# Performance work log

Measured on AMD Instinct MI355X. Metric: run time of the kernel, lower is better.

Reference implementation:

```python
import jax, jax.numpy as jnp
import numpy as np

N = 100000   # nodes
E = 1600000  # edges (avg degree 16)
D = 64       # input_dim
H = 64       # hidden_dim
C = 40       # num_classes
K = 2        # x_steps (KProp)


def setup_inputs() -> dict:
    key = jax.random.key(0)
    ks = jax.random.split(key, 8)
    x = jax.random.normal(ks[0], (N, D), dtype=jnp.float32)
    edge_src = jax.random.randint(ks[1], (E,), 0, N, dtype=jnp.int32)
    edge_dst = jax.random.randint(ks[2], (E,), 0, N, dtype=jnp.int32)
    def lin(k, fi, fo):
        b = 1.0 / np.sqrt(fi)
        return jax.random.uniform(k, (fi, fo), jnp.float32, -b, b)
    Wl1 = lin(ks[3], D, H)  # SAGEConv1 neighbor weight
    Wr1 = lin(ks[4], D, H)  # SAGEConv1 root weight
    b1 = jnp.zeros((H,), jnp.float32)
    Wl2 = lin(ks[5], H, C)
    Wr2 = lin(ks[6], H, C)
    b2 = jnp.zeros((C,), jnp.float32)
    return {"x": x, "Wl1": Wl1, "Wr1": Wr1, "b1": b1,
            "Wl2": Wl2, "Wr2": Wr2, "b2": b2,
            "edge_src": edge_src, "edge_dst": edge_dst}


def reference(x, Wl1, Wr1, b1, Wl2, Wr2, b2, edge_src, edge_dst):
    ones = jnp.ones((edge_src.shape[0],), x.dtype)
    deg = jax.ops.segment_sum(ones, edge_dst, num_segments=N)  # in-degree (adj_t row sums)
    # gcn_norm without self loops: w_e = deg[dst]^-1/2 * deg[src]^-1/2 (inf -> 0)
    dis = jnp.where(deg > 0, jax.lax.rsqrt(jnp.maximum(deg, 1.0)), 0.0)
    w = dis[edge_dst] * dis[edge_src]
    # KProp: K steps of normalized sparse matmul, 'add' aggregation
    h = x
    for _ in range(K):
        h = jax.ops.segment_sum(h[edge_src] * w[:, None], edge_dst, num_segments=N)
    cnt = jnp.maximum(deg, 1.0)[:, None]  # mean-aggr denominator (0-row safe)
    # SAGEConv1: lin_l(mean_neighbors) + lin_r(root), then selu (dropout p=0)
    agg1 = jax.ops.segment_sum(h[edge_src], edge_dst, num_segments=N) / cnt
    h1 = jax.nn.selu(agg1 @ Wl1 + h @ Wr1 + b1)
    # SAGEConv2
    agg2 = jax.ops.segment_sum(h1[edge_src], edge_dst, num_segments=N) / cnt
    out = agg2 @ Wl2 + h1 @ Wr2 + b2
    return jax.nn.softmax(out, axis=1)
```

## Files before the change

kernel.cpp:

```cpp
#include <hip/hip_runtime.h>
#include <hip/hip_bf16.h>
#include <math.h>


#define RFL(x) __builtin_amdgcn_readfirstlane(x)
#define BK_SHIFT 10
#define MAXBUCK 256

__device__ __forceinline__ float bf2f(unsigned short u) {
    return __uint_as_float((unsigned)u << 16);
}


__global__ void init_bcursor_kernel(int* __restrict__ bcursor, int nbuck, int cap) {
    int i = blockIdx.x * blockDim.x + threadIdx.x;
    if (i < nbuck) bcursor[i] = i * cap;
}

__global__ __launch_bounds__(256) void partition_kernel(const int* __restrict__ src,
                                                        const int* __restrict__ dst,
                                                        int* __restrict__ bcursor,
                                                        unsigned int* __restrict__ temp,
                                                        int e, int nbuck, int cap) {
    __shared__ int bc[MAXBUCK];
    int t = threadIdx.x;
    int chunk = (e + gridDim.x - 1) / gridDim.x;
    int base = blockIdx.x * chunk;
    int cnt = e - base;
    if (cnt > chunk) cnt = chunk;
    if (cnt < 0) cnt = 0;
    for (int j = t; j < nbuck; j += 256) bc[j] = 0;
    __syncthreads();
    for (int i = t; i < cnt; i += 256) {
        int d = dst[base + i];
        atomicAdd(&bc[d >> BK_SHIFT], 1);
    }
    __syncthreads();
    for (int j = t; j < nbuck; j += 256) {
        int c = bc[j];
        bc[j] = (c > 0) ? atomicAdd(&bcursor[j], c) : 0;
    }
    __syncthreads();
    for (int i = t; i < cnt; i += 256) {
        int s = src[base + i];
        int d = dst[base + i];
        int bk = d >> BK_SHIFT;
        int p = atomicAdd(&bc[bk], 1);
        if (p < (bk + 1) * cap) temp[p] = ((unsigned int)s << BK_SHIFT) | (unsigned int)(d & 1023);
    }
}

__global__ __launch_bounds__(256) void bucket_csr_kernel(const unsigned int* __restrict__ temp,
                                                         const int* __restrict__ bcursor,
                                                         int* __restrict__ row_ptr,
                                                         float* __restrict__ dis,
                                                         float* __restrict__ cnt_inv,
                                                         int* __restrict__ csr_src,
                                                         int n, int cap, int nbuck, int e) {
    __shared__ int cnt3[1024];
    __shared__ int part[256];
    int b = blockIdx.x;
    int t = threadIdx.x;
    int nbeg = b << BK_SHIFT;
    int cj = 0;
    if (t < nbuck) {
        cj = bcursor[t] - t * cap;
        if (cj > cap) cj = cap;
    }
    part[t] = cj;
    __syncthreads();
    for (int off = 1; off < 256; off <<= 1) {
        int u = (t >= off) ? part[t - off] : 0;
        __syncthreads();
        part[t] += u;
        __syncthreads();
    }
    int cntb = bcursor[b] - b * cap;
    if (cntb > cap) cntb = cap;
    int bbase = part[b] - cntb;
    __syncthreads();
    for (int i = t; i < 1024; i += 256) cnt3[i] = 0;
    __syncthreads();
    const unsigned int* tb = temp + (size_t)b * cap;
    for (int i = t; i < cntb; i += 256) {
        atomicAdd(&cnt3[tb[i] & 1023u], 1);
    }
    __syncthreads();
    int d0 = cnt3[t * 4 + 0], d1 = cnt3[t * 4 + 1], d2 = cnt3[t * 4 + 2], d3 = cnt3[t * 4 + 3];
    int run = d0 + d1 + d2 + d3;
    int dd[4] = {d0, d1, d2, d3};
#pragma unroll
    for (int k = 0; k < 4; ++k) {
        int node = nbeg + t * 4 + k;
        if (node < n) {
            float fd = (float)dd[k];
            dis[node] = (dd[k] > 0) ? rsqrtf(fd) : 0.0f;
            cnt_inv[node] = 1.0f / fmaxf(fd, 1.0f);
        }
    }
    __syncthreads();
    part[t] = run;
    __syncthreads();
    for (int off = 1; off < 256; off <<= 1) {
        int u = (t >= off) ? part[t - off] : 0;
        __syncthreads();
        part[t] += u;
        __syncthreads();
    }
    int ex = part[t] - run;
    int oo[4];
    oo[0] = ex; oo[1] = ex + d0; oo[2] = ex + d0 + d1; oo[3] = ex + d0 + d1 + d2;
#pragma unroll
    for (int k = 0; k < 4; ++k) {
        cnt3[t * 4 + k] = oo[k];
        int node = nbeg + t * 4 + k;
        if (node < n) row_ptr[node] = bbase + oo[k];
    }
    if (b == nbuck - 1 && t == 0) row_ptr[n] = e;
    __syncthreads();
    for (int i = t; i < cntb; i += 256) {
        unsigned int ed = tb[i];
        int pos = atomicAdd(&cnt3[ed & 1023u], 1);
        csr_src[bbase + pos] = (int)(ed >> BK_SHIFT);
    }
}

template <int TAG>
__global__ __launch_bounds__(256) void prop4_kernel(const float4* __restrict__ in4,
                                                    float4* __restrict__ out4,
                                                    const int* __restrict__ row_ptr,
                                                    const int* __restrict__ csr_src,
                                                    const float* __restrict__ dis,
                                                    int n) {
    int lane = threadIdx.x & 63;
    int g = lane >> 4;
    int l = lane & 15;
    int node = RFL(blockIdx.x * 4 + (threadIdx.x >> 6));
    if (node >= n) return;
    int beg = row_ptr[node];
    int end = row_ptr[node + 1];
    float4 acc = make_float4(0.f, 0.f, 0.f, 0.f);
    int j = beg;
    for (; j + 16 <= end; j += 16) {
        int s[4];
        float4 v[4];
        float w[4];
#pragma unroll
        for (int q = 0; q < 4; ++q) s[q] = csr_src[j + q * 4 + g];
#pragma unroll
        for (int q = 0; q < 4; ++q) v[q] = in4[(size_t)s[q] * 16 + l];
#pragma unroll
        for (int q = 0; q < 4; ++q) w[q] = dis[s[q]];
#pragma unroll
        for (int q = 0; q < 4; ++q) {
            acc.x += w[q] * v[q].x;
            acc.y += w[q] * v[q].y;
            acc.z += w[q] * v[q].z;
            acc.w += w[q] * v[q].w;
        }
    }
    for (; j + 8 <= end; j += 8) {
        int s[2];
        float4 v[2];
        float w[2];
#pragma unroll
        for (int q = 0; q < 2; ++q) s[q] = csr_src[j + q * 4 + g];
#pragma unroll
        for (int q = 0; q < 2; ++q) v[q] = in4[(size_t)s[q] * 16 + l];
#pragma unroll
        for (int q = 0; q < 2; ++q) w[q] = dis[s[q]];
#pragma unroll
        for (int q = 0; q < 2; ++q) {
            acc.x += w[q] * v[q].x;
            acc.y += w[q] * v[q].y;
            acc.z += w[q] * v[q].z;
            acc.w += w[q] * v[q].w;
        }
    }
    for (; j < end; j += 4) {
        int idx = j + g;
        bool valid = idx < end;
        int s = csr_src[valid ? idx : (end - 1)];
        float w = valid ? dis[s] : 0.0f;
        float4 v = in4[(size_t)s * 16 + l];
        acc.x += w * v.x;
        acc.y += w * v.y;
        acc.z += w * v.z;
        acc.w += w * v.w;
    }
    acc.x += __shfl_xor(acc.x, 16); acc.x += __shfl_xor(acc.x, 32);
    acc.y += __shfl_xor(acc.y, 16); acc.y += __shfl_xor(acc.y, 32);
    acc.z += __shfl_xor(acc.z, 16); acc.z += __shfl_xor(acc.z, 32);
    acc.w += __shfl_xor(acc.w, 16); acc.w += __shfl_xor(acc.w, 32);
    if (g == 0) {
        float sc = dis[node];
        out4[(size_t)node * 16 + l] = make_float4(acc.x * sc, acc.y * sc, acc.z * sc, acc.w * sc);
    }
}

__global__ __launch_bounds__(256) void prop_mean_bf_kernel(const ushort4* __restrict__ in4u,
                                                           float4* __restrict__ out4,
                                                           const int* __restrict__ row_ptr,
                                                           const int* __restrict__ csr_src,
                                                           const float* __restrict__ cnt_inv,
                                                           const float4* __restrict__ r4,
                                                           const float4* __restrict__ b4,
                                                           int n) {
    int lane = threadIdx.x & 63;
    int g = lane >> 4;
    int l = lane & 15;
    int node = RFL(blockIdx.x * 4 + (threadIdx.x >> 6));
    if (node >= n) return;
    int beg = row_ptr[node];
    int end = row_ptr[node + 1];
    float4 acc = make_float4(0.f, 0.f, 0.f, 0.f);
    int j = beg;
    for (; j + 16 <= end; j += 16) {
        int s[4];
        ushort4 u[4];
#pragma unroll
        for (int q = 0; q < 4; ++q) s[q] = csr_src[j + q * 4 + g];
#pragma unroll
        for (int q = 0; q < 4; ++q) u[q] = in4u[(size_t)s[q] * 16 + l];
#pragma unroll
        for (int q = 0; q < 4; ++q) {
            acc.x += bf2f(u[q].x);
            acc.y += bf2f(u[q].y);
            acc.z += bf2f(u[q].z);
            acc.w += bf2f(u[q].w);
        }
    }
    for (; j + 8 <= end; j += 8) {
        int s[2];
        ushort4 u[2];
#pragma unroll
        for (int q = 0; q < 2; ++q) s[q] = csr_src[j + q * 4 + g];
#pragma unroll
        for (int q = 0; q < 2; ++q) u[q] = in4u[(size_t)s[q] * 16 + l];
#pragma unroll
        for (int q = 0; q < 2; ++q) {
            acc.x += bf2f(u[q].x);
            acc.y += bf2f(u[q].y);
            acc.z += bf2f(u[q].z);
            acc.w += bf2f(u[q].w);
        }
    }
    for (; j < end; j += 4) {
        int idx = j + g;
        bool valid = idx < end;
        int s = csr_src[valid ? idx : (end - 1)];
        float w = valid ? 1.0f : 0.0f;
        ushort4 u = in4u[(size_t)s * 16 + l];
        acc.x += w * bf2f(u.x);
        acc.y += w * bf2f(u.y);
        acc.z += w * bf2f(u.z);
        acc.w += w * bf2f(u.w);
    }
    acc.x += __shfl_xor(acc.x, 16); acc.x += __shfl_xor(acc.x, 32);
    acc.y += __shfl_xor(acc.y, 16); acc.y += __shfl_xor(acc.y, 32);
    acc.z += __shfl_xor(acc.z, 16); acc.z += __shfl_xor(acc.z, 32);
    acc.w += __shfl_xor(acc.w, 16); acc.w += __shfl_xor(acc.w, 32);
    if (g == 0) {
        float sc = cnt_inv[node];
        float4 ra = r4[(size_t)node * 16 + l];
        float4 bb = b4[l];
        const float scale = 1.0507009873554805f;
        const float alpha = 1.6732632423543772f;
        float t0 = acc.x * sc + ra.x + bb.x;
        float t1 = acc.y * sc + ra.y + bb.y;
        float t2 = acc.z * sc + ra.z + bb.z;
        float t3 = acc.w * sc + ra.w + bb.w;
        float4 r;
        r.x = scale * (t0 > 0.0f ? t0 : alpha * expm1f(t0));
        r.y = scale * (t1 > 0.0f ? t1 : alpha * expm1f(t1));
        r.z = scale * (t2 > 0.0f ? t2 : alpha * expm1f(t2));
        r.w = scale * (t3 > 0.0f ? t3 : alpha * expm1f(t3));
        out4[(size_t)node * 16 + l] = r;
    }
}

__global__ __launch_bounds__(256) void prop_softmax_bf_kernel(const unsigned short* __restrict__ in_bf,
                                                              float* __restrict__ out,
                                                              const int* __restrict__ row_ptr,
                                                              const int* __restrict__ csr_src,
                                                              const float* __restrict__ cnt_inv,
                                                              const float* __restrict__ r_add,
                                                              int n) {
    int lane = threadIdx.x & 63;
    int node = RFL(blockIdx.x * 4 + (threadIdx.x >> 6));
    if (node >= n) return;
    int beg = row_ptr[node];
    int end = row_ptr[node + 1];
    float acc = 0.0f;
    int j = beg;
    for (; j + 16 <= end; j += 16) {
        int s[16];
        unsigned short v[16];
#pragma unroll
        for (int q = 0; q < 16; ++q) s[q] = csr_src[j + q];
#pragma unroll
        for (int q = 0; q < 16; ++q) v[q] = in_bf[(size_t)s[q] * 40 + lane];
#pragma unroll
        for (int q = 0; q < 16; ++q) acc += bf2f(v[q]);
    }
    for (; j + 8 <= end; j += 8) {
        int s[8];
        unsigned short v[8];
#pragma unroll
        for (int q = 0; q < 8; ++q) s[q] = csr_src[j + q];
#pragma unroll
        for (int q = 0; q < 8; ++q) v[q] = in_bf[(size_t)s[q] * 40 + lane];
#pragma unroll
        for (int q = 0; q < 8; ++q) acc += bf2f(v[q]);
    }
    for (; j < end; ++j) {
        acc += bf2f(in_bf[(size_t)csr_src[j] * 40 + lane]);
    }
    float t = acc * cnt_inv[node] + ((lane < 40) ? r_add[(size_t)node * 40 + lane] : 0.0f);
    float x = (lane < 40) ? t : -INFINITY;
    float m = x;
    for (int off = 32; off; off >>= 1) m = fmaxf(m, __shfl_xor(m, off));
    float e = (lane < 40) ? __expf(x - m) : 0.0f;
    float s = e;
    for (int off = 32; off; off >>= 1) s += __shfl_xor(s, off);
    if (lane < 40) out[(size_t)node * 40 + lane] = e / s;
}

template <int OC, int CP>
__global__ __launch_bounds__(256) void gemm_kernel(const float* __restrict__ in,
                                                   const float* __restrict__ Wl,
                                                   const float* __restrict__ Wr,
                                                   const float* __restrict__ bias,
                                                   __hip_bfloat16* __restrict__ outL,
                                                   float* __restrict__ outR,
                                                   int n, int add_bias) {
    constexpr int HC = OC / 2;
    constexpr int TX = OC / CP;
    constexpr int TY = 256 / TX;
    constexpr int NPT = 64 / TY;
    constexpr int XP = 68;
    constexpr int WP = OC + 4;
    __shared__ float sXT[64 * XP];
    __shared__ float sW[64 * WP];
    int t = threadIdx.x;
    int blk = blockIdx.x;
    for (int i = 0; i < 16; ++i) {
        int idx = i * 256 + t;
        int nd = idx >> 6;
        int k = idx & 63;
        int ng = blk * 64 + nd;
        float v = in[(size_t)(ng < n ? ng : n - 1) * 64 + k];
        sXT[k * XP + nd] = v;
    }
    for (int i = t; i < 64 * HC; i += 256) {
        int k = i / HC;
        int c = i % HC;
        sW[k * WP + c] = Wl[i];
        sW[k * WP + HC + c] = Wr[i];
    }
    __syncthreads();
    int tx = t % TX;
    int ty = t / TX;
    float acc[NPT][CP];
#pragma unroll
    for (int i = 0; i < NPT; ++i)
#pragma unroll
        for (int c = 0; c < CP; ++c) acc[i][c] = 0.0f;
#pragma unroll 4
    for (int k = 0; k < 64; ++k) {
        float xv[NPT];
#pragma unroll
        for (int i = 0; i < NPT; ++i) xv[i] = sXT[k * XP + ty * NPT + i];
        float wv[CP];
#pragma unroll
        for (int c = 0; c < CP; ++c) wv[c] = sW[k * WP + tx + TX * c];
#pragma unroll
        for (int i = 0; i < NPT; ++i)
#pragma unroll
            for (int c = 0; c < CP; ++c) acc[i][c] += xv[i] * wv[c];
    }
#pragma unroll
    for (int i = 0; i < NPT; ++i) {
        int ng = blk * 64 + ty * NPT + i;
        if (ng >= n) break;
#pragma unroll
        for (int c = 0; c < CP; ++c) {
            int col = tx + TX * c;
            if (col < HC) {
                outL[(size_t)ng * HC + col] = __float2bfloat16(acc[i][c]);
            } else {
                float v = acc[i][c] + (add_bias ? bias[col - HC] : 0.0f);
                outR[(size_t)ng * HC + (col - HC)] = v;
            }
        }
    }
}


extern "C" void kernel_launch(void* const* d_in, const int* in_sizes, int n_in,
                              void* d_out, int out_size, void* d_ws, size_t ws_size,
                              hipStream_t stream) {
    const float* x   = (const float*)d_in[0];
    const float* Wl1 = (const float*)d_in[1];
    const float* Wr1 = (const float*)d_in[2];
    const float* b1  = (const float*)d_in[3];
    const float* Wl2 = (const float*)d_in[4];
    const float* Wr2 = (const float*)d_in[5];
    const float* b2  = (const float*)d_in[6];
    const int* edge_src = (const int*)d_in[7];
    const int* edge_dst = (const int*)d_in[8];
    float* out = (float*)d_out;

    const int N = in_sizes[0] / 64;
    const int E = in_sizes[7];
    const int NBUCK = (N + (1 << BK_SHIFT) - 1) >> BK_SHIFT;
    size_t bufC_bytes = (size_t)N * 64 * 4;
    int cap = E / NBUCK + E / (2 * NBUCK) + 1024;
    int cap_max = (int)(bufC_bytes / ((size_t)NBUCK * 4));
    if (cap > cap_max) cap = cap_max;

    size_t off = 0;
    auto carve = [&](size_t bytes) -> void* {
        void* p = (char*)d_ws + off;
        off = (off + bytes + 255) & ~(size_t)255;
        return p;
    };
    int*          row_ptr = (int*)carve((size_t)(N + 1) * 4);
    int*          bcursor = (int*)carve((size_t)NBUCK * 4);
    float*        dis     = (float*)carve((size_t)N * 4);
    float*        cnt_inv = (float*)carve((size_t)N * 4);
    int*          csr_src = (int*)carve((size_t)E * 4);
    float*        bufA    = (float*)carve((size_t)N * 64 * 4);
    float*        bufB    = (float*)carve((size_t)N * 64 * 4);
    float*        bufC    = (float*)carve(bufC_bytes);
    unsigned int* temp    = (unsigned int*)bufC;
    (void)ws_size;

    const int nb_node = (N + 3) / 4;
    const int nb_gemm = (N + 63) / 64;

    init_bcursor_kernel<<<(NBUCK + 255) / 256, 256, 0, stream>>>(bcursor, NBUCK, cap);
    partition_kernel<<<256, 256, 0, stream>>>(edge_src, edge_dst, bcursor, temp, E, NBUCK, cap);
    bucket_csr_kernel<<<NBUCK, 256, 0, stream>>>(temp, bcursor, row_ptr, dis, cnt_inv,
                                                 csr_src, N, cap, NBUCK, E);

    prop4_kernel<1><<<nb_node, 256, 0, stream>>>((const float4*)x, (float4*)bufA,
                                                 row_ptr, csr_src, dis, N);
    prop4_kernel<2><<<nb_node, 256, 0, stream>>>((const float4*)bufA, (float4*)bufB,
                                                 row_ptr, csr_src, dis, N);
    gemm_kernel<128, 8><<<nb_gemm, 256, 0, stream>>>(bufB, Wl1, Wr1, nullptr,
                                                     (__hip_bfloat16*)bufA, bufC, N, 0);
    prop_mean_bf_kernel<<<nb_node, 256, 0, stream>>>((const ushort4*)bufA, (float4*)bufB,
                                                     row_ptr, csr_src, cnt_inv,
                                                     (const float4*)bufC, (const float4*)b1, N);
    gemm_kernel<80, 5><<<nb_gemm, 256, 0, stream>>>(bufB, Wl2, Wr2, b2,
                                                    (__hip_bfloat16*)bufA, bufC, N, 1);
    prop_softmax_bf_kernel<<<nb_node, 256, 0, stream>>>((const unsigned short*)bufA, out,
                                                        row_ptr, csr_src, cnt_inv, bufC, N);
}
```

Measured before the change: 434.4 us.

## Store KProp features and hidden activations in bf16 to halve gather traffic

Adds a kernel that converts x to bf16, then runs both KProp propagation steps on bf16 inputs and outputs with fp32 accumulation. The SELU output and the GEMM inputs also become bf16, and the workspace buffers are re-carved into half-size regions. The aim is to halve the bytes moved in the memory-bound neighbor gathers and the GEMM loads. In exchange it adds a conversion pass and extra rounding error compounded over several propagation steps, which could exceed the tolerance.

```diff
diff --git a/kernel.cpp b/kernel.cpp
--- a/kernel.cpp
+++ b/kernel.cpp
@@ -9,6 +9,10 @@
 
 __device__ __forceinline__ float bf2f(unsigned short u) {
     return __uint_as_float((unsigned)u << 16);
+}
+__device__ __forceinline__ unsigned short f2bf(float f) {
+    __hip_bfloat16 b = __float2bfloat16(f);
+    return *reinterpret_cast<unsigned short*>(&b);
 }
 
 
@@ -125,13 +129,23 @@
     }
 }
 
+__global__ void f2bf_kernel(const float4* __restrict__ in, ushort4* __restrict__ out, int n4) {
+    int i = blockIdx.x * blockDim.x + threadIdx.x;
+    if (i < n4) {
+        float4 v = in[i];
+        ushort4 u;
+        u.x = f2bf(v.x); u.y = f2bf(v.y); u.z = f2bf(v.z); u.w = f2bf(v.w);
+        out[i] = u;
+    }
+}
+
 template <int TAG>
-__global__ __launch_bounds__(256) void prop4_kernel(const float4* __restrict__ in4,
-                                                    float4* __restrict__ out4,
-                                                    const int* __restrict__ row_ptr,
-                                                    const int* __restrict__ csr_src,
-                                                    const float* __restrict__ dis,
-                                                    int n) {
+__global__ __launch_bounds__(256) void prop4bf_kernel(const ushort4* __restrict__ in4u,
+                                                      ushort4* __restrict__ out4u,
+                                                      const int* __restrict__ row_ptr,
+                                                      const int* __restrict__ csr_src,
+                                                      const float* __restrict__ dis,
+                                                      int n) {
     int lane = threadIdx.x & 63;
     int g = lane >> 4;
     int l = lane & 15;
@@ -143,38 +157,38 @@
     int j = beg;
     for (; j + 16 <= end; j += 16) {
         int s[4];
-        float4 v[4];
+        ushort4 u[4];
         float w[4];
 #pragma unroll
         for (int q = 0; q < 4; ++q) s[q] = csr_src[j + q * 4 + g];
 #pragma unroll
-        for (int q = 0; q < 4; ++q) v[q] = in4[(size_t)s[q] * 16 + l];
+        for (int q = 0; q < 4; ++q) u[q] = in4u[(size_t)s[q] * 16 + l];
 #pragma unroll
         for (int q = 0; q < 4; ++q) w[q] = dis[s[q]];
 #pragma unroll
         for (int q = 0; q < 4; ++q) {
-            acc.x += w[q] * v[q].x;
-            acc.y += w[q] * v[q].y;
-            acc.z += w[q] * v[q].z;
-            acc.w += w[q] * v[q].w;
+            acc.x += w[q] * bf2f(u[q].x);
+            acc.y += w[q] * bf2f(u[q].y);
+            acc.z += w[q] * bf2f(u[q].z);
+            acc.w += w[q] * bf2f(u[q].w);
         }
     }
     for (; j + 8 <= end; j += 8) {
         int s[2];
-        float4 v[2];
+        ushort4 u[2];
         float w[2];
 #pragma unroll
         for (int q = 0; q < 2; ++q) s[q] = csr_src[j + q * 4 + g];
 #pragma unroll
-        for (int q = 0; q < 2; ++q) v[q] = in4[(size_t)s[q] * 16 + l];
+        for (int q = 0; q < 2; ++q) u[q] = in4u[(size_t)s[q] * 16 + l];
 #pragma unroll
         for (int q = 0; q < 2; ++q) w[q] = dis[s[q]];
 #pragma unroll
         for (int q = 0; q < 2; ++q) {
-            acc.x += w[q] * v[q].x;
-            acc.y += w[q] * v[q].y;
-            acc.z += w[q] * v[q].z;
-            acc.w += w[q] * v[q].w;
+            acc.x += w[q] * bf2f(u[q].x);
+            acc.y += w[q] * bf2f(u[q].y);
+            acc.z += w[q] * bf2f(u[q].z);
+            acc.w += w[q] * bf2f(u[q].w);
         }
     }
     for (; j < end; j += 4) {
@@ -182,11 +196,11 @@
         bool valid = idx < end;
         int s = csr_src[valid ? idx : (end - 1)];
         float w = valid ? dis[s] : 0.0f;
-        float4 v = in4[(size_t)s * 16 + l];
-        acc.x += w * v.x;
-        acc.y += w * v.y;
-        acc.z += w * v.z;
-        acc.w += w * v.w;
+        ushort4 u = in4u[(size_t)s * 16 + l];
+        acc.x += w * bf2f(u.x);
+        acc.y += w * bf2f(u.y);
+        acc.z += w * bf2f(u.z);
+        acc.w += w * bf2f(u.w);
     }
     acc.x += __shfl_xor(acc.x, 16); acc.x += __shfl_xor(acc.x, 32);
     acc.y += __shfl_xor(acc.y, 16); acc.y += __shfl_xor(acc.y, 32);
@@ -194,12 +208,17 @@
     acc.w += __shfl_xor(acc.w, 16); acc.w += __shfl_xor(acc.w, 32);
     if (g == 0) {
         float sc = dis[node];
-        out4[(size_t)node * 16 + l] = make_float4(acc.x * sc, acc.y * sc, acc.z * sc, acc.w * sc);
+        ushort4 o;
+        o.x = f2bf(acc.x * sc);
+        o.y = f2bf(acc.y * sc);
+        o.z = f2bf(acc.z * sc);
+        o.w = f2bf(acc.w * sc);
+        out4u[(size_t)node * 16 + l] = o;
     }
 }
 
 __global__ __launch_bounds__(256) void prop_mean_bf_kernel(const ushort4* __restrict__ in4u,
-                                                           float4* __restrict__ out4,
+                                                           ushort4* __restrict__ out4u,
                                                            const int* __restrict__ row_ptr,
                                                            const int* __restrict__ csr_src,
                                                            const float* __restrict__ cnt_inv,
@@ -270,12 +289,13 @@
         float t1 = acc.y * sc + ra.y + bb.y;
         float t2 = acc.z * sc + ra.z + bb.z;
         float t3 = acc.w * sc + ra.w + bb.w;
-        float4 r;
-        r.x = scale * (t0 > 0.0f ? t0 : alpha * expm1f(t0));
-        r.y = scale * (t1 > 0.0f ? t1 : alpha * expm1f(t1));
-        r.z = scale * (t2 > 0.0f ? t2 : alpha * expm1f(t2));
-        r.w = scale * (t3 > 0.0f ? t3 : alpha * expm1f(t3));
-        out4[(size_t)node * 16 + l] = r;
+        t0 = scale * (t0 > 0.0f ? t0 : alpha * expm1f(t0));
+        t1 = scale * (t1 > 0.0f ? t1 : alpha * expm1f(t1));
+        t2 = scale * (t2 > 0.0f ? t2 : alpha * expm1f(t2));
+        t3 = scale * (t3 > 0.0f ? t3 : alpha * expm1f(t3));
+        ushort4 o;
+        o.x = f2bf(t0); o.y = f2bf(t1); o.z = f2bf(t2); o.w = f2bf(t3);
+        out4u[(size_t)node * 16 + l] = o;
     }
 }
 
@@ -327,7 +347,7 @@
 }
 
 template <int OC, int CP>
-__global__ __launch_bounds__(256) void gemm_kernel(const float* __restrict__ in,
+__global__ __launch_bounds__(256) void gemm_kernel(const unsigned short* __restrict__ in,
                                                    const float* __restrict__ Wl,
                                                    const float* __restrict__ Wr,
                                                    const float* __restrict__ bias,
@@ -349,7 +369,7 @@
         int nd = idx >> 6;
         int k = idx & 63;
         int ng = blk * 64 + nd;
-        float v = in[(size_t)(ng < n ? ng : n - 1) * 64 + k];
+        float v = bf2f(in[(size_t)(ng < n ? ng : n - 1) * 64 + k]);
         sXT[k * XP + nd] = v;
     }
     for (int i = t; i < 64 * HC; i += 256) {
@@ -414,9 +434,9 @@
     const int N = in_sizes[0] / 64;
     const int E = in_sizes[7];
     const int NBUCK = (N + (1 << BK_SHIFT) - 1) >> BK_SHIFT;
-    size_t bufC_bytes = (size_t)N * 64 * 4;
+    size_t buf_bytes = (size_t)N * 64 * 4;
     int cap = E / NBUCK + E / (2 * NBUCK) + 1024;
-    int cap_max = (int)(bufC_bytes / ((size_t)NBUCK * 4));
+    int cap_max = (int)(buf_bytes / ((size_t)NBUCK * 4));
     if (cap > cap_max) cap = cap_max;
 
     size_t off = 0;
@@ -430,31 +450,40 @@
     float*        dis     = (float*)carve((size_t)N * 4);
     float*        cnt_inv = (float*)carve((size_t)N * 4);
     int*          csr_src = (int*)carve((size_t)E * 4);
-    float*        bufA    = (float*)carve((size_t)N * 64 * 4);
-    float*        bufB    = (float*)carve((size_t)N * 64 * 4);
-    float*        bufC    = (float*)carve(bufC_bytes);
+    char*         bufA    = (char*)carve(buf_bytes);
+    char*         bufB    = (char*)carve(buf_bytes);
+    float*        bufC    = (float*)carve(buf_bytes);
     unsigned int* temp    = (unsigned int*)bufC;
     (void)ws_size;
 
+    unsigned short* xb  = (unsigned short*)bufA;
+    unsigned short* p0b = (unsigned short*)(bufA + buf_bytes / 2);
+    unsigned short* hb  = (unsigned short*)bufB;
+    unsigned short* t1b = (unsigned short*)bufA;
+    unsigned short* h1b = (unsigned short*)bufB;
+    unsigned short* t2b = (unsigned short*)(bufA + buf_bytes / 2);
+
     const int nb_node = (N + 3) / 4;
     const int nb_gemm = (N + 63) / 64;
+    const int n4 = N * 64 / 4;
 
     init_bcursor_kernel<<<(NBUCK + 255) / 256, 256, 0, stream>>>(bcursor, NBUCK, cap);
     partition_kernel<<<256, 256, 0, stream>>>(edge_src, edge_dst, bcursor, temp, E, NBUCK, cap);
     bucket_csr_kernel<<<NBUCK, 256, 0, stream>>>(temp, bcursor, row_ptr, dis, cnt_inv,
                                                  csr_src, N, cap, NBUCK, E);
 
-    prop4_kernel<1><<<nb_node, 256, 0, stream>>>((const float4*)x, (float4*)bufA,
-                                                 row_ptr, csr_src, dis, N);
-    prop4_kernel<2><<<nb_node, 256, 0, stream>>>((const float4*)bufA, (float4*)bufB,
-                                                 row_ptr, csr_src, dis, N);
-    gemm_kernel<128, 8><<<nb_gemm, 256, 0, stream>>>(bufB, Wl1, Wr1, nullptr,
-                                                     (__hip_bfloat16*)bufA, bufC, N, 0);
-    prop_mean_bf_kernel<<<nb_node, 256, 0, stream>>>((const ushort4*)bufA, (float4*)bufB,
+    f2bf_kernel<<<(n4 + 255) / 256, 256, 0, stream>>>((const float4*)x, (ushort4*)xb, n4);
+    prop4bf_kernel<1><<<nb_node, 256, 0, stream>>>((const ushort4*)xb, (ushort4*)p0b,
+                                                   row_ptr, csr_src, dis, N);
+    prop4bf_kernel<2><<<nb_node, 256, 0, stream>>>((const ushort4*)p0b, (ushort4*)hb,
+                                                   row_ptr, csr_src, dis, N);
+    gemm_kernel<128, 8><<<nb_gemm, 256, 0, stream>>>(hb, Wl1, Wr1, nullptr,
+                                                     (__hip_bfloat16*)t1b, bufC, N, 0);
+    prop_mean_bf_kernel<<<nb_node, 256, 0, stream>>>((const ushort4*)t1b, (ushort4*)h1b,
                                                      row_ptr, csr_src, cnt_inv,
                                                      (const float4*)bufC, (const float4*)b1, N);
-    gemm_kernel<80, 5><<<nb_gemm, 256, 0, stream>>>(bufB, Wl2, Wr2, b2,
-                                                    (__hip_bfloat16*)bufA, bufC, N, 1);
-    prop_softmax_bf_kernel<<<nb_node, 256, 0, stream>>>((const unsigned short*)bufA, out,
-                                                        row_ptr, csr_src, cnt_inv, bufC, N);
-}
+    gemm_kernel<80, 5><<<nb_gemm, 256, 0, stream>>>(h1b, Wl2, Wr2, b2,
+                                                    (__hip_bfloat16*)t2b, bufC, N, 1);
+    prop_softmax_bf_kernel<<<nb_node, 256, 0, stream>>>(t2b, out, row_ptr, csr_src,
+                                                        cnt_inv, bufC, N);
+}
```

After: 399.4 us. 1.09x faster.
